# Kernel optimization log

Hardware: AMD Instinct MI355X
Metric: run time of the kernel (lower is better)

The kernel has to match this reference:

```python
import jax, jax.numpy as jnp
import numpy as np

BATCH, SEQ, N_INPUT, N_HIDDEN, N_OUTPUT = 256, 512, 512, 128, 2


def setup_inputs() -> dict:
    key = jax.random.key(0)
    ks = jax.random.split(key, 6)
    s_i = 1.0 / np.sqrt(N_INPUT)
    s_h = 1.0 / np.sqrt(N_HIDDEN)
    return {
        "x": jax.random.normal(ks[0], (BATCH, SEQ, N_INPUT), dtype=jnp.float32),
        # LSTM gate kernels, gate order (i, f, g, o) concatenated on last axis.
        # flax nn.LSTMCell: dense_i has no bias, dense_h has bias.
        "Wi": jax.random.normal(ks[1], (N_INPUT, 4 * N_HIDDEN), dtype=jnp.float32) * s_i,
        "Wh": jax.random.normal(ks[2], (N_HIDDEN, 4 * N_HIDDEN), dtype=jnp.float32) * s_h,
        "b": jax.random.normal(ks[3], (4 * N_HIDDEN,), dtype=jnp.float32) * 0.01,
        "Wd": jax.random.normal(ks[4], (N_HIDDEN, N_OUTPUT), dtype=jnp.float32) * s_h,
        "bd": jax.random.normal(ks[5], (N_OUTPUT,), dtype=jnp.float32) * 0.01,
    }


def reference(x, Wi, Wh, b, Wd, bd):
    B, S, _ = x.shape
    H = Wh.shape[0]
    # Precompute input projection for all steps in one big GEMM: (S, B, 4H)
    x_gates = jnp.einsum('bsi,ig->sbg', x, Wi)

    def step(carry, xg):
        c, h = carry
        gates = xg + h @ Wh + b  # (B, 4H)
        i, f, g, o = jnp.split(gates, 4, axis=-1)
        c = jax.nn.sigmoid(f) * c + jax.nn.sigmoid(i) * jnp.tanh(g)
        h = jax.nn.sigmoid(o) * jnp.tanh(c)
        return (c, h), h

    c0 = jnp.zeros((B, H), dtype=x.dtype)
    h0 = jnp.zeros((B, H), dtype=x.dtype)
    (_, h_last), _ = jax.lax.scan(step, (c0, h0), x_gates)
    logits = h_last @ Wd + bd  # (B, N_OUTPUT)
    return logits
```

## Files before the change

kernel.cpp:

```cpp
#include <hip/hip_runtime.h>
#include <hip/hip_bf16.h>


typedef __attribute__((ext_vector_type(8))) short short8;
typedef __attribute__((ext_vector_type(4))) float floatx4;
typedef __attribute__((ext_vector_type(4))) unsigned short ushortx4;
typedef __attribute__((ext_vector_type(2))) unsigned int uint2v;

#define LOG2E 1.44269504088896340736f

__device__ __forceinline__ unsigned short f2bf(float f) {
  unsigned int u = __builtin_bit_cast(unsigned int, f);
  u = (u + 0x7fffu + ((u >> 16) & 1u)) >> 16;
  return (unsigned short)u;
}
__device__ __forceinline__ float bf2f(unsigned short u) {
  unsigned int v = ((unsigned int)u) << 16;
  return __builtin_bit_cast(float, v);
}
__device__ __forceinline__ float sigf(float x) {
  return __builtin_amdgcn_rcpf(1.0f + __builtin_amdgcn_exp2f(-LOG2E * x));
}
__device__ __forceinline__ float tanhf_(float x) {
  return 1.0f - 2.0f * __builtin_amdgcn_rcpf(1.0f + __builtin_amdgcn_exp2f(2.0f * LOG2E * x));
}
__device__ __forceinline__ void bar_lds() {
  asm volatile("s_waitcnt lgkmcnt(0)" ::: "memory");
  __builtin_amdgcn_s_barrier();
  __builtin_amdgcn_sched_barrier(0);
}
__device__ __forceinline__ void gl_lds16(const void* g, void* l) {
  __builtin_amdgcn_global_load_lds(
      (const __attribute__((address_space(1))) unsigned int*)g,
      (__attribute__((address_space(3))) unsigned int*)l, 16, 0, 0);
}

__global__ void pack_kernel(const float* __restrict__ Wi, const float* __restrict__ Wh,
                            unsigned short* __restrict__ Wi_p, unsigned short* __restrict__ Wh_p,
                            unsigned int* __restrict__ flags) {
  if (blockIdx.x == 0 && threadIdx.x < 8) flags[threadIdx.x] = 0u;
  int idx = blockIdx.x * 256 + threadIdx.x;
  if (idx < 262144) {
    int j = idx & 7, lane = (idx >> 3) & 63, nt = (idx >> 9) & 31, kk = idx >> 14;
    int k = kk * 32 + ((lane >> 4) * 8) + j;
    int n = nt * 16 + (lane & 15);
    Wi_p[idx] = f2bf(Wi[k * 512 + n]);
  } else {
    int i2 = idx - 262144;
    int j = i2 & 7, lane = (i2 >> 3) & 63, nt = (i2 >> 9) & 31, kk = i2 >> 14;
    int k = kk * 32 + ((lane >> 4) * 8) + j;
    int n = nt * 16 + (lane & 15);
    Wh_p[i2] = f2bf(Wh[k * 512 + n]);
  }
}

__global__ __launch_bounds__(512, 2) void fused_kernel(
    const float* __restrict__ x, const unsigned short* __restrict__ Wi_p,
    const float* __restrict__ bias, unsigned int* __restrict__ xg5,
    const unsigned short* __restrict__ Wh_p, const float* __restrict__ Wd,
    const float* __restrict__ bd, float* __restrict__ out,
    unsigned int* __restrict__ flags) {
  __shared__ __align__(16) unsigned short As[128 * 72];
  __shared__ __align__(16) unsigned short Bs[2 * 32 * 64 * 8];
  __shared__ __align__(16) unsigned short hb[2 * 16 * 140];
  __shared__ __align__(16) float gbw[8 * 320];

  const int tid = threadIdx.x;
  const int lane = tid & 63;
  const int w = tid >> 6;
  const int quad = lane >> 4;
  const int lm = lane & 15;

  if (blockIdx.x < 192) {
    const int wm = w >> 2, wn = w & 3;

    float bs_[4][2];
    #pragma unroll
    for (int g = 0; g < 4; ++g)
      #pragma unroll
      for (int jc = 0; jc < 2; ++jc)
        bs_[g][jc] = bias[g * 128 + wn * 32 + jc * 16 + lm];

    for (int t = blockIdx.x; t < 1024; t += 192) {
      const int s = t >> 1;
      const int b0 = (t & 1) * 128;

      floatx4 acc[4][8];
      #pragma unroll
      for (int a = 0; a < 4; ++a)
        #pragma unroll
        for (int b2 = 0; b2 < 8; ++b2) { acc[a][b2].x = 0.f; acc[a][b2].y = 0.f; acc[a][b2].z = 0.f; acc[a][b2].w = 0.f; }

      const float* xbase = x + ((size_t)(b0 + w * 16 + quad) * 512 + s) * 512 + lm * 4;

      floatx4 cur[4], nxt[4];
      #pragma unroll
      for (int i = 0; i < 4; ++i)
        cur[i] = *(const floatx4*)(xbase + (size_t)i * 1048576);

      for (int kt = 0; kt < 8; ++kt) {
        bar_lds();
        #pragma unroll
        for (int i = 0; i < 4; ++i) {
          int r = w * 16 + i * 4 + quad;
          ushortx4 u;
          u.x = f2bf(cur[i].x); u.y = f2bf(cur[i].y); u.z = f2bf(cur[i].z); u.w = f2bf(cur[i].w);
          *(ushortx4*)(&As[r * 72 + lm * 4]) = u;
        }
        #pragma unroll
        for (int c = 0; c < 8; ++c) {
          int kg = c & 1, ntl = (c >> 1) * 8 + w;
          const unsigned short* src = Wi_p + ((size_t)((kt * 2 + kg) * 32 + ntl) * 64 + lane) * 8;
          unsigned short* dst = &Bs[(size_t)((kg * 32 + ntl) * 64) * 8];
          gl_lds16(src, dst);
        }
        __builtin_amdgcn_sched_barrier(0);
        if (kt < 7) {
          #pragma unroll
          for (int i = 0; i < 4; ++i)
            nxt[i] = *(const floatx4*)(xbase + (size_t)i * 1048576 + (kt + 1) * 64);
          asm volatile("s_waitcnt vmcnt(4) lgkmcnt(0)" ::: "memory");
        } else {
          asm volatile("s_waitcnt vmcnt(0) lgkmcnt(0)" ::: "memory");
        }
        __builtin_amdgcn_s_barrier();
        __builtin_amdgcn_sched_barrier(0);
        #pragma unroll
        for (int ks = 0; ks < 2; ++ks) {
          short8 af[4];
          #pragma unroll
          for (int mt = 0; mt < 4; ++mt) {
            int m = wm * 64 + mt * 16 + lm;
            af[mt] = *(const short8*)(&As[m * 72 + ks * 32 + quad * 8]);
          }
          #pragma unroll
          for (int nt = 0; nt < 8; ++nt) {
            int g = nt >> 1, jc = nt & 1;
            int ntl = g * 8 + wn * 2 + jc;
            short8 bfv = *(const short8*)(&Bs[(size_t)((ks * 32 + ntl) * 64 + lane) * 8]);
            #pragma unroll
            for (int mt = 0; mt < 4; ++mt)
              acc[mt][nt] = __builtin_amdgcn_mfma_f32_16x16x32_bf16(af[mt], bfv, acc[mt][nt], 0, 0, 0);
          }
        }
        #pragma unroll
        for (int i = 0; i < 4; ++i) cur[i] = nxt[i];
      }
      #pragma unroll
      for (int mt = 0; mt < 4; ++mt) {
        int bbase = b0 + wm * 64 + mt * 16 + quad * 4;
        #pragma unroll
        for (int jc = 0; jc < 2; ++jc) {
          int wv = wn * 2 + jc;
          #pragma unroll
          for (int rr = 0; rr < 4; ++rr) {
            size_t cell = ((size_t)s * 64 + ((bbase + rr) >> 2)) * 512 + wv * 64 + rr * 16 + lm;
            float g0 = acc[mt][0 + jc][rr] + bs_[0][jc];
            float g1 = acc[mt][2 + jc][rr] + bs_[1][jc];
            float g2 = acc[mt][4 + jc][rr] + bs_[2][jc];
            float g3 = acc[mt][6 + jc][rr] + bs_[3][jc];
            unsigned long long v64 =
                (unsigned long long)((unsigned int)f2bf(g0) | ((unsigned int)f2bf(g1) << 16)) |
                ((unsigned long long)((unsigned int)f2bf(g2) | ((unsigned int)f2bf(g3) << 16)) << 32);
            __hip_atomic_store((unsigned long long*)xg5 + cell, v64,
                               __ATOMIC_RELAXED, __HIP_MEMORY_SCOPE_AGENT);
          }
        }
      }
      __syncthreads();
      __builtin_amdgcn_sched_barrier(0);
      if (tid == 0)
        __hip_atomic_fetch_add(&flags[t >> 7], 1u, __ATOMIC_RELEASE, __HIP_MEMORY_SCOPE_AGENT);
    }
  } else {
    const int bb = blockIdx.x - 192;

    for (int i = tid; i < 2 * 16 * 140; i += 512) hb[i] = 0;

    short8 bfr[4][4];
    #pragma unroll
    for (int kk = 0; kk < 4; ++kk)
      #pragma unroll
      for (int g = 0; g < 4; ++g)
        bfr[kk][g] = *(const short8*)(Wh_p + ((size_t)(kk * 32 + g * 8 + w) * 64 + lane) * 8);

    float cst = 0.f;

    const unsigned long long* xp = (const unsigned long long*)xg5 + ((size_t)bb * 512 + tid);
    float* gw = gbw + w * 320;

    auto at_load8 = [](const unsigned long long* p) -> uint2v {
      unsigned long long v = __hip_atomic_load(p, __ATOMIC_RELAXED, __HIP_MEMORY_SCOPE_AGENT);
      uint2v r; r.x = (unsigned int)v; r.y = (unsigned int)(v >> 32); return r;
    };

    __syncthreads();

    uint2v xga, xgb;

    auto substep = [&](const int rp, uint2v& xcur, int spre) {
      uint2v xv = xcur;
      if (spre < 512)
        xcur = at_load8(xp + (size_t)spre * 32768);

      short8 af[4];
      #pragma unroll
      for (int kk = 0; kk < 4; ++kk) {
        const unsigned short* p = &hb[rp * 2240 + lm * 140 + kk * 32 + quad * 8];
        union { short8 v; ushortx4 h[2]; } t;
        t.h[0] = *(const ushortx4*)(p);
        t.h[1] = *(const ushortx4*)(p + 4);
        af[kk] = t.v;
      }
      floatx4 acc[4];
      #pragma unroll
      for (int g = 0; g < 4; ++g) { acc[g].x = 0.f; acc[g].y = 0.f; acc[g].z = 0.f; acc[g].w = 0.f; }
      #pragma unroll
      for (int kk = 0; kk < 4; ++kk)
        #pragma unroll
        for (int g = 0; g < 4; ++g)
          acc[g] = __builtin_amdgcn_mfma_f32_16x16x32_bf16(af[kk], bfr[kk][g], acc[g], 0, 0, 0);

      if (lane < 16) {
        #pragma unroll
        for (int r = 0; r < 4; ++r) {
          floatx4 t4;
          t4.x = acc[0][r]; t4.y = acc[1][r]; t4.z = acc[2][r]; t4.w = acc[3][r];
          *(floatx4*)(gw + lm * 20 + r * 4) = t4;
        }
      }
      asm volatile("s_waitcnt lgkmcnt(0)" ::: "memory");
      __builtin_amdgcn_sched_barrier(0);
      floatx4 gv = *(const floatx4*)(gw + lm * 20 + quad * 4);

      float pre0 = gv.x + bf2f((unsigned short)(xv.x & 0xffffu));
      float pre1 = gv.y + bf2f((unsigned short)(xv.x >> 16));
      float pre2 = gv.z + bf2f((unsigned short)(xv.y & 0xffffu));
      float pre3 = gv.w + bf2f((unsigned short)(xv.y >> 16));
      float cc = sigf(pre1) * cst + sigf(pre0) * tanhf_(pre2);
      cst = cc;
      float hv = sigf(pre3) * tanhf_(cc);
      hb[(rp ^ 1) * 2240 + quad * 140 + w * 16 + lm] = f2bf(hv);
      bar_lds();
    };

    for (int c = 0; c < 8; ++c) {
      if (w == 0) {
        while (__hip_atomic_load(&flags[c], __ATOMIC_RELAXED, __HIP_MEMORY_SCOPE_AGENT) < 128u)
          __builtin_amdgcn_s_sleep(2);
      }
      bar_lds();
      xga = at_load8(xp + (size_t)(c * 64) * 32768);
      xgb = at_load8(xp + (size_t)(c * 64 + 1) * 32768);
      #pragma unroll 1
      for (int s2 = 0; s2 < 64; s2 += 2) {
        int s = c * 64 + s2;
        substep(0, xga, s + 2);
        substep(1, xgb, s + 3);
      }
    }

    if (tid < 8) {
      int rw = tid >> 1, co = tid & 1;
      float a = bd[co];
      for (int j2 = 0; j2 < 128; ++j2)
        a += bf2f(hb[rw * 140 + j2]) * Wd[j2 * 2 + co];
      out[(bb * 4 + rw) * 2 + co] = a;
    }
  }
}

extern "C" void kernel_launch(void* const* d_in, const int* in_sizes, int n_in,
                              void* d_out, int out_size, void* d_ws, size_t ws_size,
                              hipStream_t stream) {
  const float* x  = (const float*)d_in[0];
  const float* Wi = (const float*)d_in[1];
  const float* Wh = (const float*)d_in[2];
  const float* b  = (const float*)d_in[3];
  const float* Wd = (const float*)d_in[4];
  const float* bd = (const float*)d_in[5];
  float* out = (float*)d_out;

  unsigned short* Wi_p = (unsigned short*)d_ws;
  unsigned short* Wh_p = Wi_p + 262144;
  unsigned int*   flags = (unsigned int*)(Wh_p + 65536);
  unsigned int*   xg5  = flags + 128;

  pack_kernel<<<1280, 256, 0, stream>>>(Wi, Wh, Wi_p, Wh_p, flags);
  fused_kernel<<<256, 512, 0, stream>>>(x, Wi_p, b, xg5, Wh_p, Wd, bd, out, flags);
}
```

Baseline: 686.4 us.

## Process two batch groups per recurrence block and add more GEMM producer blocks

```diff
diff --git a/kernel.cpp b/kernel.cpp
--- a/kernel.cpp
+++ b/kernel.cpp
@@ -8,6 +8,7 @@
 typedef __attribute__((ext_vector_type(2))) unsigned int uint2v;
 
 #define LOG2E 1.44269504088896340736f
+#define NPROD 224
 
 __device__ __forceinline__ unsigned short f2bf(float f) {
   unsigned int u = __builtin_bit_cast(unsigned int, f);
@@ -62,8 +63,8 @@
     unsigned int* __restrict__ flags) {
   __shared__ __align__(16) unsigned short As[128 * 72];
   __shared__ __align__(16) unsigned short Bs[2 * 32 * 64 * 8];
-  __shared__ __align__(16) unsigned short hb[2 * 16 * 140];
-  __shared__ __align__(16) float gbw[8 * 320];
+  __shared__ __align__(16) unsigned short hb[4 * 2240];
+  __shared__ __align__(16) float gbw[8 * 640];
 
   const int tid = threadIdx.x;
   const int lane = tid & 63;
@@ -71,7 +72,7 @@
   const int quad = lane >> 4;
   const int lm = lane & 15;
 
-  if (blockIdx.x < 192) {
+  if (blockIdx.x < NPROD) {
     const int wm = w >> 2, wn = w & 3;
 
     float bs_[4][2];
@@ -81,7 +82,7 @@
       for (int jc = 0; jc < 2; ++jc)
         bs_[g][jc] = bias[g * 128 + wn * 32 + jc * 16 + lm];
 
-    for (int t = blockIdx.x; t < 1024; t += 192) {
+    for (int t = blockIdx.x; t < 1024; t += NPROD) {
       const int s = t >> 1;
       const int b0 = (t & 1) * 128;
 
@@ -173,9 +174,9 @@
         __hip_atomic_fetch_add(&flags[t >> 7], 1u, __ATOMIC_RELEASE, __HIP_MEMORY_SCOPE_AGENT);
     }
   } else {
-    const int bb = blockIdx.x - 192;
-
-    for (int i = tid; i < 2 * 16 * 140; i += 512) hb[i] = 0;
+    const int bb = blockIdx.x - NPROD;
+
+    for (int i = tid; i < 4 * 2240; i += 512) hb[i] = 0;
 
     short8 bfr[4][4];
     #pragma unroll
@@ -184,10 +185,12 @@
       for (int g = 0; g < 4; ++g)
         bfr[kk][g] = *(const short8*)(Wh_p + ((size_t)(kk * 32 + g * 8 + w) * 64 + lane) * 8);
 
-    float cst = 0.f;
-
-    const unsigned long long* xp = (const unsigned long long*)xg5 + ((size_t)bb * 512 + tid);
-    float* gw = gbw + w * 320;
+    float cstA = 0.f, cstB = 0.f;
+
+    const unsigned long long* xpA = (const unsigned long long*)xg5 + ((size_t)(2 * bb) * 512 + tid);
+    const unsigned long long* xpB = (const unsigned long long*)xg5 + ((size_t)(2 * bb + 1) * 512 + tid);
+    float* gwA = gbw + w * 640;
+    float* gwB = gbw + w * 640 + 320;
 
     auto at_load8 = [](const unsigned long long* p) -> uint2v {
       unsigned long long v = __hip_atomic_load(p, __ATOMIC_RELAXED, __HIP_MEMORY_SCOPE_AGENT);
@@ -196,51 +199,84 @@
 
     __syncthreads();
 
-    uint2v xga, xgb;
-
-    auto substep = [&](const int rp, uint2v& xcur, int spre) {
-      uint2v xv = xcur;
-      if (spre < 512)
-        xcur = at_load8(xp + (size_t)spre * 32768);
-
-      short8 af[4];
+    uint2v xgaA, xgbA, xgaB, xgbB;
+
+    auto substep = [&](const int rp, uint2v& xcA, uint2v& xcB, int spre) {
+      uint2v xvA = xcA, xvB = xcB;
+      if (spre < 512) {
+        xcA = at_load8(xpA + (size_t)spre * 32768);
+        xcB = at_load8(xpB + (size_t)spre * 32768);
+      }
+
+      short8 afA[4], afB[4];
       #pragma unroll
       for (int kk = 0; kk < 4; ++kk) {
-        const unsigned short* p = &hb[rp * 2240 + lm * 140 + kk * 32 + quad * 8];
-        union { short8 v; ushortx4 h[2]; } t;
-        t.h[0] = *(const ushortx4*)(p);
-        t.h[1] = *(const ushortx4*)(p + 4);
-        af[kk] = t.v;
-      }
-      floatx4 acc[4];
-      #pragma unroll
-      for (int g = 0; g < 4; ++g) { acc[g].x = 0.f; acc[g].y = 0.f; acc[g].z = 0.f; acc[g].w = 0.f; }
+        const unsigned short* pA = &hb[rp * 2240 + lm * 140 + kk * 32 + quad * 8];
+        union { short8 v; ushortx4 h[2]; } tA, tB;
+        tA.h[0] = *(const ushortx4*)(pA);
+        tA.h[1] = *(const ushortx4*)(pA + 4);
+        tB.h[0] = *(const ushortx4*)(pA + 4480);
+        tB.h[1] = *(const ushortx4*)(pA + 4484);
+        afA[kk] = tA.v; afB[kk] = tB.v;
+      }
+
+      floatx4 accA[4], accB[4];
+      #pragma unroll
+      for (int g = 0; g < 4; ++g) {
+        accA[g].x = 0.f; accA[g].y = 0.f; accA[g].z = 0.f; accA[g].w = 0.f;
+        accB[g].x = 0.f; accB[g].y = 0.f; accB[g].z = 0.f; accB[g].w = 0.f;
+      }
       #pragma unroll
       for (int kk = 0; kk < 4; ++kk)
         #pragma unroll
         for (int g = 0; g < 4; ++g)
-          acc[g] = __builtin_amdgcn_mfma_f32_16x16x32_bf16(af[kk], bfr[kk][g], acc[g], 0, 0, 0);
-
+          accA[g] = __builtin_amdgcn_mfma_f32_16x16x32_bf16(afA[kk], bfr[kk][g], accA[g], 0, 0, 0);
       if (lane < 16) {
         #pragma unroll
         for (int r = 0; r < 4; ++r) {
           floatx4 t4;
-          t4.x = acc[0][r]; t4.y = acc[1][r]; t4.z = acc[2][r]; t4.w = acc[3][r];
-          *(floatx4*)(gw + lm * 20 + r * 4) = t4;
+          t4.x = accA[0][r]; t4.y = accA[1][r]; t4.z = accA[2][r]; t4.w = accA[3][r];
+          *(floatx4*)(gwA + lm * 20 + r * 4) = t4;
+        }
+      }
+      #pragma unroll
+      for (int kk = 0; kk < 4; ++kk)
+        #pragma unroll
+        for (int g = 0; g < 4; ++g)
+          accB[g] = __builtin_amdgcn_mfma_f32_16x16x32_bf16(afB[kk], bfr[kk][g], accB[g], 0, 0, 0);
+      if (lane < 16) {
+        #pragma unroll
+        for (int r = 0; r < 4; ++r) {
+          floatx4 t4;
+          t4.x = accB[0][r]; t4.y = accB[1][r]; t4.z = accB[2][r]; t4.w = accB[3][r];
+          *(floatx4*)(gwB + lm * 20 + r * 4) = t4;
         }
       }
       asm volatile("s_waitcnt lgkmcnt(0)" ::: "memory");
       __builtin_amdgcn_sched_barrier(0);
-      floatx4 gv = *(const floatx4*)(gw + lm * 20 + quad * 4);
-
-      float pre0 = gv.x + bf2f((unsigned short)(xv.x & 0xffffu));
-      float pre1 = gv.y + bf2f((unsigned short)(xv.x >> 16));
-      float pre2 = gv.z + bf2f((unsigned short)(xv.y & 0xffffu));
-      float pre3 = gv.w + bf2f((unsigned short)(xv.y >> 16));
-      float cc = sigf(pre1) * cst + sigf(pre0) * tanhf_(pre2);
-      cst = cc;
-      float hv = sigf(pre3) * tanhf_(cc);
-      hb[(rp ^ 1) * 2240 + quad * 140 + w * 16 + lm] = f2bf(hv);
+      floatx4 gvA = *(const floatx4*)(gwA + lm * 20 + quad * 4);
+      floatx4 gvB = *(const floatx4*)(gwB + lm * 20 + quad * 4);
+
+      {
+        float pre0 = gvA.x + bf2f((unsigned short)(xvA.x & 0xffffu));
+        float pre1 = gvA.y + bf2f((unsigned short)(xvA.x >> 16));
+        float pre2 = gvA.z + bf2f((unsigned short)(xvA.y & 0xffffu));
+        float pre3 = gvA.w + bf2f((unsigned short)(xvA.y >> 16));
+        float cc = sigf(pre1) * cstA + sigf(pre0) * tanhf_(pre2);
+        cstA = cc;
+        float hv = sigf(pre3) * tanhf_(cc);
+        hb[(rp ^ 1) * 2240 + quad * 140 + w * 16 + lm] = f2bf(hv);
+      }
+      {
+        float pre0 = gvB.x + bf2f((unsigned short)(xvB.x & 0xffffu));
+        float pre1 = gvB.y + bf2f((unsigned short)(xvB.x >> 16));
+        float pre2 = gvB.z + bf2f((unsigned short)(xvB.y & 0xffffu));
+        float pre3 = gvB.w + bf2f((unsigned short)(xvB.y >> 16));
+        float cc = sigf(pre1) * cstB + sigf(pre0) * tanhf_(pre2);
+        cstB = cc;
+        float hv = sigf(pre3) * tanhf_(cc);
+        hb[4480 + (rp ^ 1) * 2240 + quad * 140 + w * 16 + lm] = f2bf(hv);
+      }
       bar_lds();
     };
 
@@ -250,22 +286,25 @@
           __builtin_amdgcn_s_sleep(2);
       }
       bar_lds();
-      xga = at_load8(xp + (size_t)(c * 64) * 32768);
-      xgb = at_load8(xp + (size_t)(c * 64 + 1) * 32768);
+      xgaA = at_load8(xpA + (size_t)(c * 64) * 32768);
+      xgbA = at_load8(xpA + (size_t)(c * 64 + 1) * 32768);
+      xgaB = at_load8(xpB + (size_t)(c * 64) * 32768);
+      xgbB = at_load8(xpB + (size_t)(c * 64 + 1) * 32768);
       #pragma unroll 1
       for (int s2 = 0; s2 < 64; s2 += 2) {
         int s = c * 64 + s2;
-        substep(0, xga, s + 2);
-        substep(1, xgb, s + 3);
+        substep(0, xgaA, xgaB, s + 2);
+        substep(1, xgbA, xgbB, s + 3);
       }
     }
 
-    if (tid < 8) {
+    if (tid < 16) {
       int rw = tid >> 1, co = tid & 1;
+      const unsigned short* hrow = (rw < 4) ? &hb[rw * 140] : &hb[4480 + (rw - 4) * 140];
       float a = bd[co];
       for (int j2 = 0; j2 < 128; ++j2)
-        a += bf2f(hb[rw * 140 + j2]) * Wd[j2 * 2 + co];
-      out[(bb * 4 + rw) * 2 + co] = a;
+        a += bf2f(hrow[j2]) * Wd[j2 * 2 + co];
+      out[(bb * 8 + rw) * 2 + co] = a;
     }
   }
 }
```

Result: slower. 936.2 us (+36.4%).
